# Performance work log

Measured on AMD Instinct MI355X. Metric: run time of the kernel, lower is better.

The kernel has to match this reference:

```python
import jax, jax.numpy as jnp
import numpy as np

N_NODES = 100000
N_EDGES = 1600000
D_IN = 64
D_HID = 64


def setup_inputs() -> dict:
    key = jax.random.key(0)
    ks = jax.random.split(key, 8)
    x = jax.random.normal(ks[0], (N_NODES, D_IN), dtype=jnp.float32)
    edge_index = jax.random.randint(ks[1], (2, N_EDGES), 0, N_NODES, dtype=jnp.int32)
    def glorot(k, fan_in, fan_out):
        s = jnp.sqrt(6.0 / (fan_in + fan_out)).astype(jnp.float32)
        return jax.random.uniform(k, (fan_in, fan_out), jnp.float32, -s, s)
    return {
        "x": x,
        "edge_index": edge_index,
        "W1": glorot(ks[2], D_IN, D_HID), "b1": jnp.zeros((D_HID,), jnp.float32),
        "W2": glorot(ks[3], D_HID, D_HID), "b2": jnp.zeros((D_HID,), jnp.float32),
        "W3": glorot(ks[4], D_HID, D_HID), "b3": jnp.zeros((D_HID,), jnp.float32),
    }


def _gcn_norm(edge_index, n_nodes):
    # add self-loops (as in PyG GCNConv default)
    loop = jnp.arange(n_nodes, dtype=edge_index.dtype)
    src = jnp.concatenate([edge_index[0], loop])
    dst = jnp.concatenate([edge_index[1], loop])
    deg = jax.ops.segment_sum(jnp.ones_like(dst, dtype=jnp.float32), dst,
                              num_segments=n_nodes)
    dinv = jnp.where(deg > 0, jax.lax.rsqrt(deg), 0.0)
    norm = dinv[src] * dinv[dst]  # [E + N]
    return src, dst, norm


def _gcn_conv(x, W, b, src, dst, norm, n_nodes):
    h = x @ W                      # [N, D] small GEMM
    msg = h[src] * norm[:, None]   # gather + scale  (memory-bound)
    out = jax.ops.segment_sum(msg, dst, num_segments=n_nodes)  # scatter-add
    return out + b


def reference(x, edge_index, W1, b1, W2, b2, W3, b3):
    n = x.shape[0]
    src, dst, norm = _gcn_norm(edge_index, n)
    h = jax.nn.relu(_gcn_conv(x, W1, b1, src, dst, norm, n))
    h = jax.nn.relu(_gcn_conv(h, W2, b2, src, dst, norm, n))
    return _gcn_conv(h, W3, b3, src, dst, norm, n)
```

## Files before the change

### kernel.cpp

```cpp
#include <hip/hip_runtime.h>
#include <hip/hip_bf16.h>

constexpr int NN  = 100000;
constexpr int NE  = 1600000;
constexpr int D   = 64;
constexpr int CAP = 64;

constexpr int NPB_SHIFT = 8;
constexpr int NBUK = (NN + 255) >> 8;
constexpr int BCAP = 4608;
constexpr int EPT  = 16;

typedef unsigned short ushort_t;
typedef unsigned int uint_t;
using short8 = __attribute__((ext_vector_type(8))) short;
using f32x4  = __attribute__((ext_vector_type(4))) float;

__device__ inline ushort_t f2bf(float f) {
    uint_t u = __float_as_uint(f);
    uint_t r = u + 0x7fffu + ((u >> 16) & 1u);
    return (ushort_t)(r >> 16);
}
__device__ inline float bflo(uint_t u) { return __uint_as_float(u << 16); }
__device__ inline float bfhi(uint_t u) { return __uint_as_float(u & 0xffff0000u); }
__device__ inline uint_t pkbf(float a, float b) {
    return (uint_t)f2bf(a) | ((uint_t)f2bf(b) << 16);
}

__global__ void k_zero(int* __restrict__ p, int n) {
    int i = blockIdx.x * blockDim.x + threadIdx.x;
    if (i < n) p[i] = 0;
}

__global__ void __launch_bounds__(256)
k_part(const int* __restrict__ src, const int* __restrict__ dst,
       int* __restrict__ bcur, uint_t* __restrict__ ebuf, int e) {
    __shared__ int hist[NBUK];
    __shared__ int base[NBUK];
    int t = threadIdx.x;
    for (int i = t; i < NBUK; i += 256) hist[i] = 0;
    __syncthreads();
    int start = blockIdx.x * (256 * EPT);
    uint_t pk[EPT];
    int bk[EPT];
#pragma unroll
    for (int i = 0; i < EPT; ++i) {
        int idx = start + i * 256 + t;
        if (idx < e) {
            int d = dst[idx];
            int b = d >> NPB_SHIFT;
            bk[i] = b;
            pk[i] = (uint_t)src[idx] | ((uint_t)(d & 255) << 17);
            atomicAdd(&hist[b], 1);
        } else bk[i] = -1;
    }
    __syncthreads();
    for (int i = t; i < NBUK; i += 256) {
        int c = hist[i];
        base[i] = (c > 0) ? atomicAdd(&bcur[i], c) : 0;
        hist[i] = 0;
    }
    __syncthreads();
#pragma unroll
    for (int i = 0; i < EPT; ++i) {
        if (bk[i] >= 0) {
            int b = bk[i];
            int r = atomicAdd(&hist[b], 1);
            int pos = base[b] + r;
            if (pos < BCAP) ebuf[(size_t)b * BCAP + pos] = pk[i];
        }
    }
}

__global__ void __launch_bounds__(256)
k_fill2(const uint_t* __restrict__ ebuf, const int* __restrict__ bcnt,
        int* __restrict__ deg, int* __restrict__ col, float* __restrict__ dinv,
        const float* __restrict__ x, ushort_t* __restrict__ xbf,
        const float* __restrict__ W1, const float* __restrict__ W2,
        const float* __restrict__ W3, ushort_t* __restrict__ wfrag) {
    int t = threadIdx.x;
    if (blockIdx.x >= NBUK) {
        int wi = blockIdx.x - NBUK;
        const float* W = (wi == 0) ? W1 : (wi == 1) ? W2 : W3;
        ushort_t* o = wfrag + wi * 4096;
        int l = t & 63;
#pragma unroll
        for (int it = 0; it < 2; ++it) {
            int f = (t >> 6) + it * 4;
            int kt = f >> 2, nt = f & 3;
            uint_t u[4];
#pragma unroll
            for (int i = 0; i < 4; ++i) {
                float a = W[(kt * 32 + (l >> 4) * 8 + 2 * i)     * 64 + nt * 16 + (l & 15)];
                float b = W[(kt * 32 + (l >> 4) * 8 + 2 * i + 1) * 64 + nt * 16 + (l & 15)];
                u[i] = pkbf(a, b);
            }
            *(uint4*)&o[(size_t)(f * 64 + l) * 8] = make_uint4(u[0], u[1], u[2], u[3]);
        }
        return;
    }
    __shared__ int cnt[256];
    __shared__ float sdv[256];
    int b = blockIdx.x;
    int n = min(bcnt[b], BCAP);
    int nbase = b << NPB_SHIFT;
    cnt[t] = 0;
    __syncthreads();
    for (int i = t; i < n; i += 256) {
        uint_t e = ebuf[(size_t)b * BCAP + i];
        int s = (int)(e & 0x1FFFFu);
        int d = (int)(e >> 17);
        int slot = atomicAdd(&cnt[d], 1);
        if (slot < CAP) col[(size_t)(nbase + d) * CAP + slot] = s;
    }
    __syncthreads();
    int nrow = min(256, NN - nbase);
    if (t < nrow) {
        int dgv = cnt[t];
        deg[nbase + t] = dgv;
        float dv = rsqrtf((float)(dgv + 1));
        dinv[nbase + t] = dv;
        sdv[t] = dv;
    }
    __syncthreads();
    for (int i = t; i < nrow * 16; i += 256) {
        int nl = i >> 4;
        float dv = sdv[nl];
        float4 v = ((const float4*)x)[(size_t)(nbase + nl) * 16 + (i & 15)];
        ((uint2*)xbf)[(size_t)(nbase + nl) * 16 + (i & 15)] =
            make_uint2(pkbf(v.x * dv, v.y * dv), pkbf(v.z * dv, v.w * dv));
    }
}

#define ACC8(u) do { \
    a0 += bflo((u).x); a1 += bfhi((u).x); a2 += bflo((u).y); a3 += bfhi((u).y); \
    a4 += bflo((u).z); a5 += bfhi((u).z); a6 += bflo((u).w); a7 += bfhi((u).w); } while (0)

template <bool RELU, bool BF16OUT>
__global__ void __launch_bounds__(256, 8)
k_layer(const ushort_t* __restrict__ xin, const int* __restrict__ col,
        const int* __restrict__ deg, const float* __restrict__ dinv,
        const ushort_t* __restrict__ wfrag, const float* __restrict__ bias,
        void* __restrict__ outv) {
    __shared__ ushort_t rowbuf[16 * D];
    __shared__ float sdv[16];
    int t = threadIdx.x, wave = t >> 6, lane = t & 63;

    int node0 = blockIdx.x * 16;
    int chain = lane >> 4;
    int c16 = lane & 48;
    int l16 = lane & 15;
    int g2  = (lane >> 3) & 1;
    int q   = lane & 7;
    const uint4* __restrict__ x4 = (const uint4*)xin;

    int n = wave * 4 + chain;
    int node = node0 + n;
    int dg = min(deg[node], CAP);
    float dv = dinv[node];
    if (l16 == 0) sdv[n] = dv;

    const int* crow = &col[(size_t)node * CAP];
    int ck0 = (l16 < dg) ? crow[l16] : 0;
    int ck1 = (16 + l16 < dg) ? crow[16 + l16] : 0;
    int ck2 = (32 + l16 < dg) ? crow[32 + l16] : 0;
    int ck3 = (48 + l16 < dg) ? crow[48 + l16] : 0;
    float a0=0.f,a1=0.f,a2=0.f,a3=0.f,a4=0.f,a5=0.f,a6=0.f,a7=0.f;

    int Gf = dg >> 3;
    for (int g = 0; g < Gf; ++g) {
        int cc = (g < 2) ? ((g < 1) ? ck0 : ck0) : (g < 4) ? ck1 : (g < 6) ? ck2 : ck3;
        if (g == 1) cc = ck0;
        int lb = c16 + ((g & 1) << 3) + g2;
        int s0 = __shfl(cc, lb);
        int s1 = __shfl(cc, lb + 2);
        int s2 = __shfl(cc, lb + 4);
        int s3 = __shfl(cc, lb + 6);
        uint4 u0 = x4[(size_t)s0 * 8 + q];
        uint4 u1 = x4[(size_t)s1 * 8 + q];
        uint4 u2 = x4[(size_t)s2 * 8 + q];
        uint4 u3 = x4[(size_t)s3 * 8 + q];
        ACC8(u0); ACC8(u1); ACC8(u2); ACC8(u3);
    }
    int rem = dg & 7;
    if (rem) {
        int g = Gf;
        int cc = (g < 2) ? ck0 : (g < 4) ? ck1 : (g < 6) ? ck2 : ck3;
        int lb = c16 + ((g & 1) << 3) + g2;
        int i0 = (g << 3) + g2;
        int s0 = __shfl(cc, lb);
        int s1 = __shfl(cc, lb + 2);
        int s2 = __shfl(cc, lb + 4);
        int s3 = __shfl(cc, lb + 6);
        uint4 u0 = x4[(size_t)s0 * 8 + q];
        uint4 u1 = x4[(size_t)s1 * 8 + q];
        uint4 u2 = x4[(size_t)s2 * 8 + q];
        uint4 u3 = x4[(size_t)s3 * 8 + q];
        uint4 z = make_uint4(0u, 0u, 0u, 0u);
        if (i0 >= dg)     u0 = z;
        if (i0 + 2 >= dg) u1 = z;
        if (i0 + 4 >= dg) u2 = z;
        if (i0 + 6 >= dg) u3 = z;
        ACC8(u0); ACC8(u1); ACC8(u2); ACC8(u3);
    }
    a0 += __shfl_xor(a0, 8); a1 += __shfl_xor(a1, 8);
    a2 += __shfl_xor(a2, 8); a3 += __shfl_xor(a3, 8);
    a4 += __shfl_xor(a4, 8); a5 += __shfl_xor(a5, 8);
    a6 += __shfl_xor(a6, 8); a7 += __shfl_xor(a7, 8);
    if (l16 < 8) {
        uint4 u = x4[(size_t)node * 8 + l16];
        a0 += bflo(u.x); a1 += bfhi(u.x); a2 += bflo(u.y); a3 += bfhi(u.y);
        a4 += bflo(u.z); a5 += bfhi(u.z); a6 += bflo(u.w); a7 += bfhi(u.w);
        uint4 p = make_uint4(pkbf(a0 * dv, a1 * dv), pkbf(a2 * dv, a3 * dv),
                             pkbf(a4 * dv, a5 * dv), pkbf(a6 * dv, a7 * dv));
        ((uint4*)rowbuf)[n * 8 + (l16 ^ (n & 7))] = p;
    }
    __syncthreads();

    short8 wfA = *(const short8*)&wfrag[(size_t)(wave * 64 + lane) * 8];
    short8 wfB = *(const short8*)&wfrag[(size_t)((4 + wave) * 64 + lane) * 8];
    float bv = bias[wave * 16 + (lane & 15)];

    int arow = lane & 15, akg = lane >> 4;
    short8 af0 = *(const short8*)&rowbuf[(size_t)arow * D + (((0 * 4 + akg) ^ (arow & 7)) * 8)];
    short8 af1 = *(const short8*)&rowbuf[(size_t)arow * D + (((4 + akg) ^ (arow & 7)) * 8)];

    f32x4 c = {bv, bv, bv, bv};
    c = __builtin_amdgcn_mfma_f32_16x16x32_bf16(af0, wfA, c, 0, 0, 0);
    c = __builtin_amdgcn_mfma_f32_16x16x32_bf16(af1, wfB, c, 0, 0, 0);

    int ccol = lane & 15, crow0 = (lane >> 4) * 4;
#pragma unroll
    for (int r = 0; r < 4; ++r) {
        int row = node0 + crow0 + r;
        float o = c[r];
        if (RELU) o = fmaxf(o, 0.f);
        if (BF16OUT) {
            float dvr = sdv[crow0 + r];
            ((ushort_t*)outv)[(size_t)row * D + wave * 16 + ccol] = f2bf(o * dvr);
        } else {
            ((float*)outv)[(size_t)row * D + wave * 16 + ccol] = o;
        }
    }
}


extern "C" void kernel_launch(void* const* d_in, const int* in_sizes, int n_in,
                              void* d_out, int out_size, void* d_ws, size_t ws_size,
                              hipStream_t stream) {
    const float* x   = (const float*)d_in[0];
    const int*   ei  = (const int*)d_in[1];
    const float* W1  = (const float*)d_in[2];
    const float* b1  = (const float*)d_in[3];
    const float* W2  = (const float*)d_in[4];
    const float* b2  = (const float*)d_in[5];
    const float* W3  = (const float*)d_in[6];
    const float* b3  = (const float*)d_in[7];
    const int* src = ei;
    const int* dst = ei + NE;
    float* out = (float*)d_out;

    int* col = (int*)d_ws;
    char* p1 = (char*)(col + (size_t)NN * CAP);
    ushort_t* xbf = (ushort_t*)p1;
    char* p2 = p1 + (size_t)NN * D * 2;
    uint_t*   ebuf = (uint_t*)p2;
    ushort_t* hbf  = (ushort_t*)p2;
    int*   deg   = (int*)(p2 + (size_t)NN * D * 2);
    int*   bcur  = deg + NN;
    float* dinv  = (float*)(deg + NN + 512);
    ushort_t* wfrag = (ushort_t*)(dinv + NN);

    k_zero<<<(NBUK + 255) / 256, 256, 0, stream>>>(bcur, NBUK);

    k_part<<<(NE + 256 * EPT - 1) / (256 * EPT), 256, 0, stream>>>(src, dst, bcur, ebuf, NE);
    k_fill2<<<NBUK + 3, 256, 0, stream>>>(ebuf, bcur, deg, col, dinv, x, xbf,
                                          W1, W2, W3, wfrag);

    int layerBlocks = NN / 16;
    k_layer<true,  true ><<<layerBlocks, 256, 0, stream>>>(xbf, col, deg, dinv, wfrag,        b1, hbf);
    k_layer<true,  true ><<<layerBlocks, 256, 0, stream>>>(hbf, col, deg, dinv, wfrag + 4096, b2, xbf);
    k_layer<false, false><<<layerBlocks, 256, 0, stream>>>(xbf, col, deg, dinv, wfrag + 8192, b3, out);
}
```

Before: 138.9 us.

## Use 32 lanes per node in layer gather and widen partition buckets

The layer kernel now runs 512 threads per block and assigns 32 lanes to each destination node instead of 16. Each lane group gathers four neighbour rows per iteration, covering 16 edges per step, and an extra cross-lane reduction combines the partial sums. Only the first four waves do the MFMA transform. Separately, partitioning moves to 512-node buckets with a larger capacity and more edges per thread, which halves the bucket count. The intent is more memory-level parallelism per node in the gather and fewer partition blocks, at the cost of idle waves during the GEMM and more wasted lanes for low-degree nodes.

```diff
diff --git a/kernel.cpp b/kernel.cpp
--- a/kernel.cpp
+++ b/kernel.cpp
@@ -6,10 +6,10 @@
 constexpr int D   = 64;
 constexpr int CAP = 64;
 
-constexpr int NPB_SHIFT = 8;
-constexpr int NBUK = (NN + 255) >> 8;
-constexpr int BCAP = 4608;
-constexpr int EPT  = 16;
+constexpr int NPB_SHIFT = 9;
+constexpr int NBUK = (NN + 511) >> 9;
+constexpr int BCAP = 9216;
+constexpr int EPT  = 25;
 
 typedef unsigned short ushort_t;
 typedef unsigned int uint_t;
@@ -50,7 +50,7 @@
             int d = dst[idx];
             int b = d >> NPB_SHIFT;
             bk[i] = b;
-            pk[i] = (uint_t)src[idx] | ((uint_t)(d & 255) << 17);
+            pk[i] = (uint_t)src[idx] | ((uint_t)(d & 511) << 17);
             atomicAdd(&hist[b], 1);
         } else bk[i] = -1;
     }
@@ -99,12 +99,12 @@
         }
         return;
     }
-    __shared__ int cnt[256];
-    __shared__ float sdv[256];
+    __shared__ int cnt[512];
+    __shared__ float sdv[512];
     int b = blockIdx.x;
     int n = min(bcnt[b], BCAP);
     int nbase = b << NPB_SHIFT;
-    cnt[t] = 0;
+    cnt[t] = 0; cnt[t + 256] = 0;
     __syncthreads();
     for (int i = t; i < n; i += 256) {
         uint_t e = ebuf[(size_t)b * BCAP + i];
@@ -114,13 +114,17 @@
         if (slot < CAP) col[(size_t)(nbase + d) * CAP + slot] = s;
     }
     __syncthreads();
-    int nrow = min(256, NN - nbase);
-    if (t < nrow) {
-        int dgv = cnt[t];
-        deg[nbase + t] = dgv;
-        float dv = rsqrtf((float)(dgv + 1));
-        dinv[nbase + t] = dv;
-        sdv[t] = dv;
+    int nrow = min(512, NN - nbase);
+#pragma unroll
+    for (int it = 0; it < 2; ++it) {
+        int i = t + it * 256;
+        if (i < nrow) {
+            int dgv = cnt[i];
+            deg[nbase + i] = dgv;
+            float dv = rsqrtf((float)(dgv + 1));
+            dinv[nbase + i] = dv;
+            sdv[i] = dv;
+        }
     }
     __syncthreads();
     for (int i = t; i < nrow * 16; i += 256) {
@@ -137,7 +141,7 @@
     a4 += bflo((u).z); a5 += bfhi((u).z); a6 += bflo((u).w); a7 += bfhi((u).w); } while (0)
 
 template <bool RELU, bool BF16OUT>
-__global__ void __launch_bounds__(256, 8)
+__global__ void __launch_bounds__(512, 8)
 k_layer(const ushort_t* __restrict__ xin, const int* __restrict__ col,
         const int* __restrict__ deg, const float* __restrict__ dinv,
         const ushort_t* __restrict__ wfrag, const float* __restrict__ bias,
@@ -145,101 +149,101 @@
     __shared__ ushort_t rowbuf[16 * D];
     __shared__ float sdv[16];
     int t = threadIdx.x, wave = t >> 6, lane = t & 63;
+    int half = lane >> 5, l32 = lane & 31;
+    int es = l32 >> 3;
+    int q  = l32 & 7;
+    int hb = half << 5;
+    const uint4* __restrict__ x4 = (const uint4*)xin;
 
     int node0 = blockIdx.x * 16;
-    int chain = lane >> 4;
-    int c16 = lane & 48;
-    int l16 = lane & 15;
-    int g2  = (lane >> 3) & 1;
-    int q   = lane & 7;
-    const uint4* __restrict__ x4 = (const uint4*)xin;
-
-    int n = wave * 4 + chain;
+    int n = wave * 2 + half;
     int node = node0 + n;
     int dg = min(deg[node], CAP);
     float dv = dinv[node];
-    if (l16 == 0) sdv[n] = dv;
+    if (l32 == 0) sdv[n] = dv;
 
     const int* crow = &col[(size_t)node * CAP];
-    int ck0 = (l16 < dg) ? crow[l16] : 0;
-    int ck1 = (16 + l16 < dg) ? crow[16 + l16] : 0;
-    int ck2 = (32 + l16 < dg) ? crow[32 + l16] : 0;
-    int ck3 = (48 + l16 < dg) ? crow[48 + l16] : 0;
+    int ck0 = (l32 < dg) ? crow[l32] : 0;
+    int ck1 = (32 + l32 < dg) ? crow[32 + l32] : 0;
     float a0=0.f,a1=0.f,a2=0.f,a3=0.f,a4=0.f,a5=0.f,a6=0.f,a7=0.f;
 
-    int Gf = dg >> 3;
-    for (int g = 0; g < Gf; ++g) {
-        int cc = (g < 2) ? ((g < 1) ? ck0 : ck0) : (g < 4) ? ck1 : (g < 6) ? ck2 : ck3;
-        if (g == 1) cc = ck0;
-        int lb = c16 + ((g & 1) << 3) + g2;
-        int s0 = __shfl(cc, lb);
-        int s1 = __shfl(cc, lb + 2);
-        int s2 = __shfl(cc, lb + 4);
-        int s3 = __shfl(cc, lb + 6);
-        uint4 u0 = x4[(size_t)s0 * 8 + q];
-        uint4 u1 = x4[(size_t)s1 * 8 + q];
-        uint4 u2 = x4[(size_t)s2 * 8 + q];
-        uint4 u3 = x4[(size_t)s3 * 8 + q];
+    int nitf = dg >> 4;
+    for (int it = 0; it < nitf; ++it) {
+        int cc = (it < 2) ? ck0 : ck1;
+        int sl = ((it & 1) << 4) + es;
+        int i0 = __shfl(cc, hb + sl);
+        int i1 = __shfl(cc, hb + sl + 4);
+        int i2 = __shfl(cc, hb + sl + 8);
+        int i3 = __shfl(cc, hb + sl + 12);
+        uint4 u0 = x4[(size_t)i0 * 8 + q];
+        uint4 u1 = x4[(size_t)i1 * 8 + q];
+        uint4 u2 = x4[(size_t)i2 * 8 + q];
+        uint4 u3 = x4[(size_t)i3 * 8 + q];
         ACC8(u0); ACC8(u1); ACC8(u2); ACC8(u3);
     }
-    int rem = dg & 7;
-    if (rem) {
-        int g = Gf;
-        int cc = (g < 2) ? ck0 : (g < 4) ? ck1 : (g < 6) ? ck2 : ck3;
-        int lb = c16 + ((g & 1) << 3) + g2;
-        int i0 = (g << 3) + g2;
-        int s0 = __shfl(cc, lb);
-        int s1 = __shfl(cc, lb + 2);
-        int s2 = __shfl(cc, lb + 4);
-        int s3 = __shfl(cc, lb + 6);
-        uint4 u0 = x4[(size_t)s0 * 8 + q];
-        uint4 u1 = x4[(size_t)s1 * 8 + q];
-        uint4 u2 = x4[(size_t)s2 * 8 + q];
-        uint4 u3 = x4[(size_t)s3 * 8 + q];
+    if (dg & 15) {
+        int it = nitf;
+        int cc = (it < 2) ? ck0 : ck1;
+        int sl = ((it & 1) << 4) + es;
+        int s0 = (it << 4) + es;
+        int i0 = __shfl(cc, hb + sl);
+        int i1 = __shfl(cc, hb + sl + 4);
+        int i2 = __shfl(cc, hb + sl + 8);
+        int i3 = __shfl(cc, hb + sl + 12);
+        uint4 u0 = x4[(size_t)i0 * 8 + q];
+        uint4 u1 = x4[(size_t)i1 * 8 + q];
+        uint4 u2 = x4[(size_t)i2 * 8 + q];
+        uint4 u3 = x4[(size_t)i3 * 8 + q];
         uint4 z = make_uint4(0u, 0u, 0u, 0u);
-        if (i0 >= dg)     u0 = z;
-        if (i0 + 2 >= dg) u1 = z;
-        if (i0 + 4 >= dg) u2 = z;
-        if (i0 + 6 >= dg) u3 = z;
+        if (s0 >= dg)      u0 = z;
+        if (s0 + 4 >= dg)  u1 = z;
+        if (s0 + 8 >= dg)  u2 = z;
+        if (s0 + 12 >= dg) u3 = z;
         ACC8(u0); ACC8(u1); ACC8(u2); ACC8(u3);
     }
-    a0 += __shfl_xor(a0, 8); a1 += __shfl_xor(a1, 8);
-    a2 += __shfl_xor(a2, 8); a3 += __shfl_xor(a3, 8);
-    a4 += __shfl_xor(a4, 8); a5 += __shfl_xor(a5, 8);
-    a6 += __shfl_xor(a6, 8); a7 += __shfl_xor(a7, 8);
-    if (l16 < 8) {
-        uint4 u = x4[(size_t)node * 8 + l16];
+    a0 += __shfl_xor(a0, 8);  a1 += __shfl_xor(a1, 8);
+    a2 += __shfl_xor(a2, 8);  a3 += __shfl_xor(a3, 8);
+    a4 += __shfl_xor(a4, 8);  a5 += __shfl_xor(a5, 8);
+    a6 += __shfl_xor(a6, 8);  a7 += __shfl_xor(a7, 8);
+    a0 += __shfl_xor(a0, 16); a1 += __shfl_xor(a1, 16);
+    a2 += __shfl_xor(a2, 16); a3 += __shfl_xor(a3, 16);
+    a4 += __shfl_xor(a4, 16); a5 += __shfl_xor(a5, 16);
+    a6 += __shfl_xor(a6, 16); a7 += __shfl_xor(a7, 16);
+    if (l32 < 8) {
+        uint4 u = x4[(size_t)node * 8 + l32];
         a0 += bflo(u.x); a1 += bfhi(u.x); a2 += bflo(u.y); a3 += bfhi(u.y);
         a4 += bflo(u.z); a5 += bfhi(u.z); a6 += bflo(u.w); a7 += bfhi(u.w);
         uint4 p = make_uint4(pkbf(a0 * dv, a1 * dv), pkbf(a2 * dv, a3 * dv),
                              pkbf(a4 * dv, a5 * dv), pkbf(a6 * dv, a7 * dv));
-        ((uint4*)rowbuf)[n * 8 + (l16 ^ (n & 7))] = p;
-    }
-    __syncthreads();
-
-    short8 wfA = *(const short8*)&wfrag[(size_t)(wave * 64 + lane) * 8];
-    short8 wfB = *(const short8*)&wfrag[(size_t)((4 + wave) * 64 + lane) * 8];
-    float bv = bias[wave * 16 + (lane & 15)];
-
-    int arow = lane & 15, akg = lane >> 4;
-    short8 af0 = *(const short8*)&rowbuf[(size_t)arow * D + (((0 * 4 + akg) ^ (arow & 7)) * 8)];
-    short8 af1 = *(const short8*)&rowbuf[(size_t)arow * D + (((4 + akg) ^ (arow & 7)) * 8)];
-
-    f32x4 c = {bv, bv, bv, bv};
-    c = __builtin_amdgcn_mfma_f32_16x16x32_bf16(af0, wfA, c, 0, 0, 0);
-    c = __builtin_amdgcn_mfma_f32_16x16x32_bf16(af1, wfB, c, 0, 0, 0);
-
-    int ccol = lane & 15, crow0 = (lane >> 4) * 4;
-#pragma unroll
-    for (int r = 0; r < 4; ++r) {
-        int row = node0 + crow0 + r;
-        float o = c[r];
-        if (RELU) o = fmaxf(o, 0.f);
-        if (BF16OUT) {
-            float dvr = sdv[crow0 + r];
-            ((ushort_t*)outv)[(size_t)row * D + wave * 16 + ccol] = f2bf(o * dvr);
-        } else {
-            ((float*)outv)[(size_t)row * D + wave * 16 + ccol] = o;
+        ((uint4*)rowbuf)[n * 8 + (l32 ^ (n & 7))] = p;
+    }
+    __syncthreads();
+
+    if (wave < 4) {
+        short8 wfA = *(const short8*)&wfrag[(size_t)(wave * 64 + lane) * 8];
+        short8 wfB = *(const short8*)&wfrag[(size_t)((4 + wave) * 64 + lane) * 8];
+        float bv = bias[wave * 16 + (lane & 15)];
+
+        int arow = lane & 15, akg = lane >> 4;
+        short8 af0 = *(const short8*)&rowbuf[(size_t)arow * D + (((0 * 4 + akg) ^ (arow & 7)) * 8)];
+        short8 af1 = *(const short8*)&rowbuf[(size_t)arow * D + (((4 + akg) ^ (arow & 7)) * 8)];
+
+        f32x4 c = {bv, bv, bv, bv};
+        c = __builtin_amdgcn_mfma_f32_16x16x32_bf16(af0, wfA, c, 0, 0, 0);
+        c = __builtin_amdgcn_mfma_f32_16x16x32_bf16(af1, wfB, c, 0, 0, 0);
+
+        int ccol = lane & 15, crow0 = (lane >> 4) * 4;
+#pragma unroll
+        for (int r = 0; r < 4; ++r) {
+            int row = node0 + crow0 + r;
+            float o = c[r];
+            if (RELU) o = fmaxf(o, 0.f);
+            if (BF16OUT) {
+                float dvr = sdv[crow0 + r];
+                ((ushort_t*)outv)[(size_t)row * D + wave * 16 + ccol] = f2bf(o * dvr);
+            } else {
+                ((float*)outv)[(size_t)row * D + wave * 16 + ccol] = o;
+            }
         }
     }
 }
@@ -271,14 +275,14 @@
     float* dinv  = (float*)(deg + NN + 512);
     ushort_t* wfrag = (ushort_t*)(dinv + NN);
 
-    k_zero<<<(NBUK + 255) / 256, 256, 0, stream>>>(bcur, NBUK);
-
-    k_part<<<(NE + 256 * EPT - 1) / (256 * EPT), 256, 0, stream>>>(src, dst, bcur, ebuf, NE);
+    k_zero<<<1, 256, 0, stream>>>(bcur, NBUK);
+
+    k_part<<<NE / (256 * EPT), 256, 0, stream>>>(src, dst, bcur, ebuf, NE);
     k_fill2<<<NBUK + 3, 256, 0, stream>>>(ebuf, bcur, deg, col, dinv, x, xbf,
                                           W1, W2, W3, wfrag);
 
     int layerBlocks = NN / 16;
-    k_layer<true,  true ><<<layerBlocks, 256, 0, stream>>>(xbf, col, deg, dinv, wfrag,        b1, hbf);
-    k_layer<true,  true ><<<layerBlocks, 256, 0, stream>>>(hbf, col, deg, dinv, wfrag + 4096, b2, xbf);
-    k_layer<false, false><<<layerBlocks, 256, 0, stream>>>(xbf, col, deg, dinv, wfrag + 8192, b3, out);
-}
+    k_layer<true,  true ><<<layerBlocks, 512, 0, stream>>>(xbf, col, deg, dinv, wfrag,        b1, hbf);
+    k_layer<true,  true ><<<layerBlocks, 512, 0, stream>>>(hbf, col, deg, dinv, wfrag + 4096, b2, xbf);
+    k_layer<false, false><<<layerBlocks, 512, 0, stream>>>(xbf, col, deg, dinv, wfrag + 8192, b3, out);
+}
```

Result: slower. 152.0 us (+9.5%).

## Sort nodes by degree so layer blocks process uniform-degree rows

Applied to the files above, without the earlier changes.

Builds a degree histogram during CSR fill, scans it, and writes a degree-sorted node permutation along with permuted degree and dinv arrays. Each layer block then handles 16 nodes of similar degree, which is meant to reduce intra-wave divergence and tail imbalance in the gather loop. Output rows are scattered through the permutation. This adds two small kernels and turns previously contiguous row reads and writes into permuted accesses.

```diff
diff --git a/kernel.cpp b/kernel.cpp
--- a/kernel.cpp
+++ b/kernel.cpp
@@ -76,6 +76,7 @@
 k_fill2(const uint_t* __restrict__ ebuf, const int* __restrict__ bcnt,
         int* __restrict__ deg, int* __restrict__ col, float* __restrict__ dinv,
         const float* __restrict__ x, ushort_t* __restrict__ xbf,
+        int* __restrict__ ghist,
         const float* __restrict__ W1, const float* __restrict__ W2,
         const float* __restrict__ W3, ushort_t* __restrict__ wfrag) {
     int t = threadIdx.x;
@@ -101,10 +102,12 @@
     }
     __shared__ int cnt[256];
     __shared__ float sdv[256];
+    __shared__ int h65[65];
     int b = blockIdx.x;
     int n = min(bcnt[b], BCAP);
     int nbase = b << NPB_SHIFT;
     cnt[t] = 0;
+    if (t < 65) h65[t] = 0;
     __syncthreads();
     for (int i = t; i < n; i += 256) {
         uint_t e = ebuf[(size_t)b * BCAP + i];
@@ -121,8 +124,10 @@
         float dv = rsqrtf((float)(dgv + 1));
         dinv[nbase + t] = dv;
         sdv[t] = dv;
-    }
-    __syncthreads();
+        atomicAdd(&h65[min(dgv, CAP)], 1);
+    }
+    __syncthreads();
+    if (t < 65 && h65[t]) atomicAdd(&ghist[t], h65[t]);
     for (int i = t; i < nrow * 16; i += 256) {
         int nl = i >> 4;
         float dv = sdv[nl];
@@ -132,21 +137,59 @@
     }
 }
 
+__global__ void k_scan(const int* __restrict__ ghist, int* __restrict__ gcur) {
+    __shared__ int s[65];
+    int t = threadIdx.x;
+    if (t < 65) s[t] = ghist[t];
+    __syncthreads();
+    if (t == 0) {
+        int acc = 0;
+        for (int i = 0; i < 65; ++i) { int v = s[i]; s[i] = acc; acc += v; }
+    }
+    __syncthreads();
+    if (t < 65) gcur[t] = s[t];
+}
+
+__global__ void __launch_bounds__(512)
+k_permf(const int* __restrict__ deg, const float* __restrict__ dinv,
+        int* __restrict__ gcur, int* __restrict__ perm,
+        int* __restrict__ pdg, float* __restrict__ pdv) {
+    __shared__ int lh[65], lb[65];
+    int t = threadIdx.x;
+    if (t < 65) lh[t] = 0;
+    __syncthreads();
+    int i = blockIdx.x * 512 + t;
+    bool v = i < NN;
+    int d = 0, r = 0;
+    if (v) { d = min(deg[i], CAP); r = atomicAdd(&lh[d], 1); }
+    __syncthreads();
+    if (t < 65) { int c = lh[t]; lb[t] = c ? atomicAdd(&gcur[t], c) : 0; }
+    __syncthreads();
+    if (v) {
+        int pos = lb[d] + r;
+        perm[pos] = i;
+        pdg[pos] = d;
+        pdv[pos] = dinv[i];
+    }
+}
+
 #define ACC8(u) do { \
     a0 += bflo((u).x); a1 += bfhi((u).x); a2 += bflo((u).y); a3 += bfhi((u).y); \
-    a4 += bflo((u).z); a5 += bfhi((u).z); a6 += bflo((u).w); a7 += bfhi((u).w); } while (0)
+    a4 += bflo((u).z); a5 += bfhi(u.z); a6 += bflo((u).w); a7 += bfhi((u).w); } while (0)
 
 template <bool RELU, bool BF16OUT>
 __global__ void __launch_bounds__(256, 8)
 k_layer(const ushort_t* __restrict__ xin, const int* __restrict__ col,
-        const int* __restrict__ deg, const float* __restrict__ dinv,
+        const int* __restrict__ perm, const int* __restrict__ pdg,
+        const float* __restrict__ pdv,
         const ushort_t* __restrict__ wfrag, const float* __restrict__ bias,
         void* __restrict__ outv) {
     __shared__ ushort_t rowbuf[16 * D];
     __shared__ float sdv[16];
+    __shared__ int sperm[16];
     int t = threadIdx.x, wave = t >> 6, lane = t & 63;
 
-    int node0 = blockIdx.x * 16;
+    int tb = blockIdx.x * 16;
     int chain = lane >> 4;
     int c16 = lane & 48;
     int l16 = lane & 15;
@@ -154,13 +197,20 @@
     int q   = lane & 7;
     const uint4* __restrict__ x4 = (const uint4*)xin;
 
+    int dgv = 0; float dvv = 0.f; int pnv = 0;
+    if (lane < 16) {
+        pnv = perm[tb + lane];
+        dgv = pdg[tb + lane];
+        dvv = pdv[tb + lane];
+        if (wave == 0) { sperm[lane] = pnv; sdv[lane] = dvv; }
+    }
+
     int n = wave * 4 + chain;
-    int node = node0 + n;
-    int dg = min(deg[node], CAP);
-    float dv = dinv[node];
-    if (l16 == 0) sdv[n] = dv;
-
-    const int* crow = &col[(size_t)node * CAP];
+    int dg = __shfl(dgv, n);
+    float dv = __shfl(dvv, n);
+    int pnode = __shfl(pnv, n);
+
+    const int* crow = &col[(size_t)pnode * CAP];
     int ck0 = (l16 < dg) ? crow[l16] : 0;
     int ck1 = (16 + l16 < dg) ? crow[16 + l16] : 0;
     int ck2 = (32 + l16 < dg) ? crow[32 + l16] : 0;
@@ -169,8 +219,7 @@
 
     int Gf = dg >> 3;
     for (int g = 0; g < Gf; ++g) {
-        int cc = (g < 2) ? ((g < 1) ? ck0 : ck0) : (g < 4) ? ck1 : (g < 6) ? ck2 : ck3;
-        if (g == 1) cc = ck0;
+        int cc = (g >= 6) ? ck3 : (g >= 4) ? ck2 : (g >= 2) ? ck1 : ck0;
         int lb = c16 + ((g & 1) << 3) + g2;
         int s0 = __shfl(cc, lb);
         int s1 = __shfl(cc, lb + 2);
@@ -182,10 +231,9 @@
         uint4 u3 = x4[(size_t)s3 * 8 + q];
         ACC8(u0); ACC8(u1); ACC8(u2); ACC8(u3);
     }
-    int rem = dg & 7;
-    if (rem) {
+    if (dg & 7) {
         int g = Gf;
-        int cc = (g < 2) ? ck0 : (g < 4) ? ck1 : (g < 6) ? ck2 : ck3;
+        int cc = (g >= 6) ? ck3 : (g >= 4) ? ck2 : (g >= 2) ? ck1 : ck0;
         int lb = c16 + ((g & 1) << 3) + g2;
         int i0 = (g << 3) + g2;
         int s0 = __shfl(cc, lb);
@@ -208,7 +256,7 @@
     a4 += __shfl_xor(a4, 8); a5 += __shfl_xor(a5, 8);
     a6 += __shfl_xor(a6, 8); a7 += __shfl_xor(a7, 8);
     if (l16 < 8) {
-        uint4 u = x4[(size_t)node * 8 + l16];
+        uint4 u = x4[(size_t)pnode * 8 + l16];
         a0 += bflo(u.x); a1 += bfhi(u.x); a2 += bflo(u.y); a3 += bfhi(u.y);
         a4 += bflo(u.z); a5 += bfhi(u.z); a6 += bflo(u.w); a7 += bfhi(u.w);
         uint4 p = make_uint4(pkbf(a0 * dv, a1 * dv), pkbf(a2 * dv, a3 * dv),
@@ -232,14 +280,14 @@
     int ccol = lane & 15, crow0 = (lane >> 4) * 4;
 #pragma unroll
     for (int r = 0; r < 4; ++r) {
-        int row = node0 + crow0 + r;
+        int prow = sperm[crow0 + r];
         float o = c[r];
         if (RELU) o = fmaxf(o, 0.f);
         if (BF16OUT) {
             float dvr = sdv[crow0 + r];
-            ((ushort_t*)outv)[(size_t)row * D + wave * 16 + ccol] = f2bf(o * dvr);
+            ((ushort_t*)outv)[(size_t)prow * D + wave * 16 + ccol] = f2bf(o * dvr);
         } else {
-            ((float*)outv)[(size_t)row * D + wave * 16 + ccol] = o;
+            ((float*)outv)[(size_t)prow * D + wave * 16 + ccol] = o;
         }
     }
 }
@@ -268,17 +316,24 @@
     ushort_t* hbf  = (ushort_t*)p2;
     int*   deg   = (int*)(p2 + (size_t)NN * D * 2);
     int*   bcur  = deg + NN;
-    float* dinv  = (float*)(deg + NN + 512);
+    int*   ghist = bcur + NBUK;
+    int*   gcur  = ghist + 65;
+    float* dinv  = (float*)(gcur + 65);
     ushort_t* wfrag = (ushort_t*)(dinv + NN);
-
-    k_zero<<<(NBUK + 255) / 256, 256, 0, stream>>>(bcur, NBUK);
+    int*   perm  = (int*)(wfrag + 3 * 4096);
+    int*   pdg   = perm + NN;
+    float* pdv   = (float*)(pdg + NN);
+
+    k_zero<<<2, 256, 0, stream>>>(bcur, NBUK + 65);
 
     k_part<<<(NE + 256 * EPT - 1) / (256 * EPT), 256, 0, stream>>>(src, dst, bcur, ebuf, NE);
-    k_fill2<<<NBUK + 3, 256, 0, stream>>>(ebuf, bcur, deg, col, dinv, x, xbf,
+    k_fill2<<<NBUK + 3, 256, 0, stream>>>(ebuf, bcur, deg, col, dinv, x, xbf, ghist,
                                           W1, W2, W3, wfrag);
+    k_scan<<<1, 128, 0, stream>>>(ghist, gcur);
+    k_permf<<<(NN + 511) / 512, 512, 0, stream>>>(deg, dinv, gcur, perm, pdg, pdv);
 
     int layerBlocks = NN / 16;
-    k_layer<true,  true ><<<layerBlocks, 256, 0, stream>>>(xbf, col, deg, dinv, wfrag,        b1, hbf);
-    k_layer<true,  true ><<<layerBlocks, 256, 0, stream>>>(hbf, col, deg, dinv, wfrag + 4096, b2, xbf);
-    k_layer<false, false><<<layerBlocks, 256, 0, stream>>>(xbf, col, deg, dinv, wfrag + 8192, b3, out);
-}
+    k_layer<true,  true ><<<layerBlocks, 256, 0, stream>>>(xbf, col, perm, pdg, pdv, wfrag,        b1, hbf);
+    k_layer<true,  true ><<<layerBlocks, 256, 0, stream>>>(hbf, col, perm, pdg, pdv, wfrag + 4096, b2, xbf);
+    k_layer<false, false><<<layerBlocks, 256, 0, stream>>>(xbf, col, perm, pdg, pdv, wfrag + 8192, b3, out);
+}
```

After: 146.7 us. +5.6%, slower.
